# Optimization experiments

Measured on AMD Instinct MI355X. Metric: run time of the kernel, lower is better.

Reference implementation:

```python
import jax, jax.numpy as jnp
import numpy as np

MP_TIMES = 3  # mp_times from init


def setup_inputs() -> dict:
    key = jax.random.key(0)
    ks = jax.random.split(key, 16)
    N, E, F, EF = 10000, 50000, 32, 16
    DL, D, G, GD, OUT = 128, 64, 256, 8, 1

    def w(k, shape, fan_in):
        return jax.random.normal(k, shape, jnp.float32) / np.float32(np.sqrt(fan_in))

    return {
        "x": jax.random.normal(ks[0], (N, F), jnp.float32),
        "edge_index": jax.random.randint(ks[1], (2, E), 0, N),
        "edge_attr": jax.random.uniform(ks[2], (E, EF), jnp.float32),
        "batch": jax.random.randint(ks[3], (N,), 0, G),
        "graph_attr": jax.random.normal(ks[4], (G, GD), jnp.float32),
        # lin0
        "W0": w(ks[5], (D, F), F), "b0": jnp.zeros((D,), jnp.float32),
        # edge network MLP: EF -> DL -> D*D
        "We1": w(ks[6], (DL, EF), EF), "be1": jnp.zeros((DL,), jnp.float32),
        "We2": w(ks[7], (D * D, DL), DL), "be2": jnp.zeros((D * D,), jnp.float32),
        # NNConv root weight + bias
        "Wroot": w(ks[8], (D, D), D), "bconv": jnp.zeros((D,), jnp.float32),
        # GRU (torch gate order: r, z, n)
        "W_ih": w(ks[9], (3 * D, D), D), "W_hh": w(ks[10], (3 * D, D), D),
        "b_ih": jnp.zeros((3 * D,), jnp.float32), "b_hh": jnp.zeros((3 * D,), jnp.float32),
        # lin1 takes cat(node_state, graph_attr) -> D  (sized D+GD to make the source's cat runnable)
        "W1": w(ks[11], (D, D + GD), D + GD), "b1": jnp.zeros((D,), jnp.float32),
        # lin2
        "W2": w(ks[12], (OUT, D), D), "b2": jnp.zeros((OUT,), jnp.float32),
    }


def reference(x, edge_index, edge_attr, batch, graph_attr,
              W0, b0, We1, be1, We2, be2, Wroot, bconv,
              W_ih, W_hh, b_ih, b_hh, W1, b1, W2, b2):
    N = x.shape[0]
    D = W0.shape[0]
    src, dst = edge_index[0], edge_index[1]

    # Per-edge weight matrices from the edge MLP (loop-invariant: edge_attr is constant).
    ew = jnp.maximum(edge_attr @ We1.T + be1, 0.0) @ We2.T + be2  # [E, D*D]
    ew = ew.reshape(-1, D, D)                                      # [E, D, D]

    # mean-aggregation denominator (isolated nodes keep 0 via max(deg,1))
    deg = jax.ops.segment_sum(jnp.ones(src.shape[0], jnp.float32), dst, num_segments=N)
    denom = jnp.maximum(deg, 1.0)[:, None]                         # [N, 1]

    out = jnp.maximum(x @ W0.T + b0, 0.0)                          # [N, D]
    h = out
    for _ in range(MP_TIMES):
        # NNConv: gather -> per-edge matmul -> scatter-mean, plus root transform
        msg = jnp.einsum('ei,eio->eo', out[src], ew)               # [E, D]
        agg = jax.ops.segment_sum(msg, dst, num_segments=N) / denom
        m = jnp.maximum(agg + out @ Wroot.T + bconv, 0.0)          # [N, D]
        # single GRU step (torch GRUCell math, gate order r,z,n)
        gi = m @ W_ih.T + b_ih
        gh = h @ W_hh.T + b_hh
        i_r, i_z, i_n = jnp.split(gi, 3, axis=-1)
        h_r, h_z, h_n = jnp.split(gh, 3, axis=-1)
        r = jax.nn.sigmoid(i_r + h_r)
        z = jax.nn.sigmoid(i_z + h_z)
        n = jnp.tanh(i_n + r * h_n)
        h = (1.0 - z) * n + z * h
        out = h

    cat = jnp.concatenate([out, graph_attr[batch]], axis=-1)       # [N, D+GD]
    hid = jnp.maximum(cat @ W1.T + b1, 0.0)
    return hid @ W2.T + b2                                         # [N, dim_output]
```

## Files before the change

### kernel.cpp

```cpp
#include <hip/hip_runtime.h>
#include <hip/hip_bf16.h>
#include <math.h>

#define FIN 32
#define EFD 16
#define GDIM 8
#define ISPLIT 2

typedef __attribute__((ext_vector_type(8))) short short8;
typedef __attribute__((ext_vector_type(4))) float f32x4;

static __device__ __forceinline__ float bf2f(unsigned short u) {
  return __uint_as_float(((unsigned)u) << 16);
}
static __device__ __forceinline__ unsigned short f2bf(float f) {
  unsigned u = __float_as_uint(f);
  unsigned r = (u + 0x7FFFu + ((u >> 16) & 1u)) >> 16;
  return (unsigned short)r;
}

__global__ void zero_f32(float* __restrict__ p, int n) {
  int i = blockIdx.x * blockDim.x + threadIdx.x;
  if (i < n) p[i] = 0.0f;
}

__global__ void deg_kernel(const int* __restrict__ dst, float* __restrict__ deg, int E) {
  int e = blockIdx.x * blockDim.x + threadIdx.x;
  if (e < E) atomicAdd(&deg[dst[e]], 1.0f);
}

__global__ void setup_fused(const float* __restrict__ ea, const float* __restrict__ We1,
                            const float* __restrict__ be1, unsigned short* __restrict__ hidden,
                            const float* __restrict__ We2, unsigned short* __restrict__ We2f,
                            const float* __restrict__ Wroot, const float* __restrict__ W_hh,
                            const float* __restrict__ be2, const float* __restrict__ W_ih,
                            unsigned short* __restrict__ Wc_fh, unsigned short* __restrict__ Wc_fl,
                            unsigned short* __restrict__ Wih_fh, unsigned short* __restrict__ Wih_fl,
                            const float* __restrict__ x, const float* __restrict__ W0,
                            const float* __restrict__ b0, float* __restrict__ state,
                            int E, int N, int eB, int cB, int pB) {
  int b = blockIdx.x;
  if (b < eB) {
    int idx = b * 256 + threadIdx.x;
    int e = idx >> 7, l = idx & 127;
    if (e >= E) return;
    float acc = be1[l];
    const float* er = ea + (size_t)e * EFD;
    const float* wr = We1 + (size_t)l * EFD;
    #pragma unroll
    for (int j = 0; j < EFD; ++j) acc += er[j] * wr[j];
    hidden[idx] = f2bf(fmaxf(acc, 0.0f));
    return;
  }
  b -= eB;
  if (b < cB) {
    int fidx = b * 256 + threadIdx.x;
    if (fidx >= 4096 * 128) return;
    int j    = fidx & 7;
    int lane = (fidx >> 3) & 63;
    int kk   = (fidx >> 9) & 3;
    int wave = (fidx >> 11) & 3;
    int i    = fidx >> 13;
    int quad = lane >> 4, col = lane & 15;
    int row  = i * 64 + wave * 16 + col;
    int cw   = kk * 32 + quad * 8 + j;
    We2f[fidx] = f2bf(We2[(size_t)row * 128 + cw]);
    return;
  }
  b -= cB;
  if (b < pB) {
    int idx = b * 256 + threadIdx.x;
    if (idx >= 20480 + 12288) return;
    if (idx < 20480) {
      int j = idx & 7, lane = (idx >> 3) & 63, kk = (idx >> 9) & 1, cgk = idx >> 10;
      int quad = lane >> 4, mcol = lane & 15;
      int wave = cgk / 5, cg = cgk % 5;
      int c = wave * 80 + cg * 16 + mcol;
      int cw = kk * 32 + quad * 8 + j;
      float w;
      if (c < 64)       w = Wroot[c * 64 + cw];
      else if (c < 256) w = W_hh[(c - 64) * 64 + cw];
      else              w = be2[cw * 64 + (c - 256)];
      unsigned short h = f2bf(w);
      Wc_fh[idx] = h;
      Wc_fl[idx] = f2bf(w - bf2f(h));
    } else {
      int t = idx - 20480;
      int j = t & 7, lane = (t >> 3) & 63, kk = (t >> 9) & 1, gw = t >> 10;
      int quad = lane >> 4, mcol = lane & 15;
      int g = gw >> 2, wave = gw & 3;
      int row = g * 64 + wave * 16 + mcol;
      int cw = kk * 32 + quad * 8 + j;
      float w = W_ih[row * 64 + cw];
      unsigned short h = f2bf(w);
      Wih_fh[t] = h;
      Wih_fl[t] = f2bf(w - bf2f(h));
    }
    return;
  }
  b -= pB;
  {
    int idx = b * 256 + threadIdx.x;
    int n = idx >> 6, d = idx & 63;
    if (n >= N) return;
    float acc = b0[d];
    const float* xr = x + (size_t)n * FIN;
    const float* wr = W0 + (size_t)d * FIN;
    #pragma unroll
    for (int f = 0; f < FIN; ++f) acc += xr[f] * wr[f];
    state[idx] = fmaxf(acc, 0.0f);
  }
}

#define MFMA(A, B, C) __builtin_amdgcn_mfma_f32_16x16x32_bf16((A), (B), (C), 0, 0, 0)

__global__ __launch_bounds__(256) void pre_kernel(const float* __restrict__ state,
    const unsigned short* __restrict__ Wc_fh, const unsigned short* __restrict__ Wc_fl,
    float* __restrict__ R, int N) {
  __shared__ __align__(16) unsigned short Sh[32 * 72], Sl[32 * 72];
  int tid = threadIdx.x;
  int n0 = blockIdx.x * 32;
  {
    int nl = tid >> 3, part = tid & 7;
    int gn = n0 + nl;
    const float* sp = state + (size_t)gn * 64 + part * 8;
    #pragma unroll
    for (int j = 0; j < 2; ++j) {
      float4 v = make_float4(0.f, 0.f, 0.f, 0.f);
      if (gn < N) v = *(const float4*)(sp + j * 4);
      int base = nl * 72 + part * 8 + j * 4;
      unsigned short h;
      h = f2bf(v.x); Sh[base + 0] = h; Sl[base + 0] = f2bf(v.x - bf2f(h));
      h = f2bf(v.y); Sh[base + 1] = h; Sl[base + 1] = f2bf(v.y - bf2f(h));
      h = f2bf(v.z); Sh[base + 2] = h; Sl[base + 2] = f2bf(v.z - bf2f(h));
      h = f2bf(v.w); Sh[base + 3] = h; Sl[base + 3] = f2bf(v.w - bf2f(h));
    }
  }
  __syncthreads();
  int lane = tid & 63, wave = tid >> 6;
  int quad = lane >> 4, mcol = lane & 15;
  short8 ah[2][2], al[2][2];
  #pragma unroll
  for (int mt = 0; mt < 2; ++mt)
    #pragma unroll
    for (int kk = 0; kk < 2; ++kk) {
      ah[mt][kk] = *(const short8*)&Sh[(mt * 16 + mcol) * 72 + kk * 32 + quad * 8];
      al[mt][kk] = *(const short8*)&Sl[(mt * 16 + mcol) * 72 + kk * 32 + quad * 8];
    }
  int c0w = wave * 80;
  #pragma unroll 1
  for (int cg = 0; cg < 5; ++cg) {
    int c = c0w + cg * 16 + mcol;
    const unsigned short* bhp = Wc_fh + (size_t)(wave * 5 + cg) * 1024 + lane * 8;
    const unsigned short* blp = Wc_fl + (size_t)(wave * 5 + cg) * 1024 + lane * 8;
    short8 bh0 = *(const short8*)bhp, bh1 = *(const short8*)(bhp + 512);
    short8 bl0 = *(const short8*)blp, bl1 = *(const short8*)(blp + 512);
    #pragma unroll
    for (int mt = 0; mt < 2; ++mt) {
      f32x4 p = (f32x4){0.f, 0.f, 0.f, 0.f};
      p = MFMA(al[mt][0], bh0, p);
      p = MFMA(ah[mt][0], bl0, p);
      p = MFMA(ah[mt][0], bh0, p);
      p = MFMA(al[mt][1], bh1, p);
      p = MFMA(ah[mt][1], bl1, p);
      p = MFMA(ah[mt][1], bh1, p);
      #pragma unroll
      for (int r = 0; r < 4; ++r) {
        int row = n0 + mt * 16 + quad * 4 + r;
        if (row < N) R[(size_t)row * 320 + c] = p[r];
      }
    }
  }
}

__global__ __launch_bounds__(256) void msg_fused(const int* __restrict__ ei,
    const float* __restrict__ state, const unsigned short* __restrict__ hidden,
    const unsigned short* __restrict__ We2f, const float* __restrict__ R,
    float* __restrict__ agg, int E) {
  __shared__ __align__(16) char smem[64 * 136 * 2];
  __shared__ int srcs[64], dsts[64];
  unsigned short* Hs = (unsigned short*)smem;
  float* St = (float*)smem;
  int tid = threadIdx.x;
  int e0 = blockIdx.x * 64;
  int i0 = blockIdx.y * 32;
  if (tid < 64) {
    int e = e0 + tid;
    srcs[tid] = (e < E) ? ei[e] : -1;
    dsts[tid] = (e < E) ? ei[E + e] : -1;
  }
  {
    int er = tid >> 2, part = tid & 3;
    int ge = e0 + er;
    const unsigned short* hp = hidden + (size_t)ge * 128 + part * 32;
    #pragma unroll
    for (int j = 0; j < 4; ++j) {
      uint4 v = make_uint4(0u, 0u, 0u, 0u);
      if (ge < E) v = *(const uint4*)(hp + j * 8);
      *(uint4*)&Hs[er * 136 + part * 32 + j * 8] = v;
    }
  }
  __syncthreads();
  int lane = tid & 63, wave = tid >> 6;
  int n0 = wave * 16;
  int quad = lane >> 4, col = lane & 15;
  short8 a[4][4];
  #pragma unroll
  for (int mt = 0; mt < 4; ++mt)
    #pragma unroll
    for (int kk = 0; kk < 4; ++kk)
      a[mt][kk] = *(const short8*)&Hs[(mt * 16 + col) * 136 + kk * 32 + quad * 8];
  float4 sreg[2];
  {
    int sn = srcs[lane];
    const float* sp = state + (size_t)(sn < 0 ? 0 : sn) * 64 + i0 + wave * 8;
    #pragma unroll
    for (int j = 0; j < 2; ++j) {
      float4 v = make_float4(0.f, 0.f, 0.f, 0.f);
      if (sn >= 0) v = *(const float4*)(sp + j * 4);
      sreg[j] = v;
    }
  }
  __syncthreads();
  #pragma unroll
  for (int j = 0; j < 2; ++j) {
    int i = wave * 8 + j * 4;
    St[(i + 0) * 64 + lane] = sreg[j].x;
    St[(i + 1) * 64 + lane] = sreg[j].y;
    St[(i + 2) * 64 + lane] = sreg[j].z;
    St[(i + 3) * 64 + lane] = sreg[j].w;
  }
  __syncthreads();

  f32x4 macc0 = (f32x4){0.f,0.f,0.f,0.f}, macc1 = (f32x4){0.f,0.f,0.f,0.f};
  f32x4 macc2 = (f32x4){0.f,0.f,0.f,0.f}, macc3 = (f32x4){0.f,0.f,0.f,0.f};
  const unsigned short* bptr = We2f + (size_t)i0 * 8192 + wave * 2048 + lane * 8;
  short8 Xa = *(const short8*)(bptr + 0);
  short8 Xb = *(const short8*)(bptr + 512);
  short8 Xc = *(const short8*)(bptr + 1024);
  short8 Xd = *(const short8*)(bptr + 1536);
  short8 Ya, Yb, Yc, Yd;
  #pragma unroll 1
  for (int ii = 0; ii < 16; ++ii) {
    int i = ii * 2;
    {
      const unsigned short* bn = bptr + (size_t)(i + 1) * 8192;
      Ya = *(const short8*)(bn + 0);
      Yb = *(const short8*)(bn + 512);
      Yc = *(const short8*)(bn + 1024);
      Yd = *(const short8*)(bn + 1536);
    }
    {
      f32x4 sv0 = *(const f32x4*)&St[i * 64 +  0 + quad * 4];
      f32x4 sv1 = *(const f32x4*)&St[i * 64 + 16 + quad * 4];
      f32x4 sv2 = *(const f32x4*)&St[i * 64 + 32 + quad * 4];
      f32x4 sv3 = *(const f32x4*)&St[i * 64 + 48 + quad * 4];
      f32x4 p0 = (f32x4){0.f,0.f,0.f,0.f}, p1 = (f32x4){0.f,0.f,0.f,0.f};
      f32x4 p2 = (f32x4){0.f,0.f,0.f,0.f}, p3 = (f32x4){0.f,0.f,0.f,0.f};
      p0 = MFMA(a[0][0], Xa, p0); p1 = MFMA(a[1][0], Xa, p1);
      p2 = MFMA(a[2][0], Xa, p2); p3 = MFMA(a[3][0], Xa, p3);
      p0 = MFMA(a[0][1], Xb, p0); p1 = MFMA(a[1][1], Xb, p1);
      p2 = MFMA(a[2][1], Xb, p2); p3 = MFMA(a[3][1], Xb, p3);
      p0 = MFMA(a[0][2], Xc, p0); p1 = MFMA(a[1][2], Xc, p1);
      p2 = MFMA(a[2][2], Xc, p2); p3 = MFMA(a[3][2], Xc, p3);
      p0 = MFMA(a[0][3], Xd, p0); p1 = MFMA(a[1][3], Xd, p1);
      p2 = MFMA(a[2][3], Xd, p2); p3 = MFMA(a[3][3], Xd, p3);
      macc0 += sv0 * p0; macc1 += sv1 * p1; macc2 += sv2 * p2; macc3 += sv3 * p3;
    }
    if (ii < 15) {
      const unsigned short* bn = bptr + (size_t)(i + 2) * 8192;
      Xa = *(const short8*)(bn + 0);
      Xb = *(const short8*)(bn + 512);
      Xc = *(const short8*)(bn + 1024);
      Xd = *(const short8*)(bn + 1536);
    }
    {
      int io = i + 1;
      f32x4 sv0 = *(const f32x4*)&St[io * 64 +  0 + quad * 4];
      f32x4 sv1 = *(const f32x4*)&St[io * 64 + 16 + quad * 4];
      f32x4 sv2 = *(const f32x4*)&St[io * 64 + 32 + quad * 4];
      f32x4 sv3 = *(const f32x4*)&St[io * 64 + 48 + quad * 4];
      f32x4 p0 = (f32x4){0.f,0.f,0.f,0.f}, p1 = (f32x4){0.f,0.f,0.f,0.f};
      f32x4 p2 = (f32x4){0.f,0.f,0.f,0.f}, p3 = (f32x4){0.f,0.f,0.f,0.f};
      p0 = MFMA(a[0][0], Ya, p0); p1 = MFMA(a[1][0], Ya, p1);
      p2 = MFMA(a[2][0], Ya, p2); p3 = MFMA(a[3][0], Ya, p3);
      p0 = MFMA(a[0][1], Yb, p0); p1 = MFMA(a[1][1], Yb, p1);
      p2 = MFMA(a[2][1], Yb, p2); p3 = MFMA(a[3][1], Yb, p3);
      p0 = MFMA(a[0][2], Yc, p0); p1 = MFMA(a[1][2], Yc, p1);
      p2 = MFMA(a[2][2], Yc, p2); p3 = MFMA(a[3][2], Yc, p3);
      p0 = MFMA(a[0][3], Yd, p0); p1 = MFMA(a[1][3], Yd, p1);
      p2 = MFMA(a[2][3], Yd, p2); p3 = MFMA(a[3][3], Yd, p3);
      macc0 += sv0 * p0; macc1 += sv1 * p1; macc2 += sv2 * p2; macc3 += sv3 * p3;
    }
  }
  int addu = (blockIdx.y == 0);
  f32x4 maccA[4] = {macc0, macc1, macc2, macc3};
  #pragma unroll
  for (int mt = 0; mt < 4; ++mt) {
    #pragma unroll
    for (int r = 0; r < 4; ++r) {
      int el = mt * 16 + quad * 4 + r;
      int d = dsts[el];
      if (d >= 0) {
        float val = maccA[mt][r];
        if (addu) val += R[(size_t)srcs[el] * 320 + 256 + n0 + col];
        atomicAdd(&agg[(size_t)d * 64 + n0 + col], val);
      }
    }
  }
}

__global__ __launch_bounds__(256) void gate_pre(float* __restrict__ agg,
    const float* __restrict__ deg, float* __restrict__ state,
    float* __restrict__ R, const float* __restrict__ bconv,
    const unsigned short* __restrict__ Wih_fh, const unsigned short* __restrict__ Wih_fl,
    const float* __restrict__ b_ih, const float* __restrict__ b_hh,
    const unsigned short* __restrict__ Wc_fh, const unsigned short* __restrict__ Wc_fl,
    int N, int do_pre) {
  __shared__ __align__(16) unsigned short Mh[32 * 72], Ml[32 * 72];
  int tid = threadIdx.x;
  int n0 = blockIdx.x * 32;
  {
    int nl = tid >> 3, part = tid & 7;
    int gn = n0 + nl;
    float inv = 1.0f;
    if (gn < N) inv = 1.0f / fmaxf(deg[gn], 1.0f);
    #pragma unroll
    for (int j = 0; j < 2; ++j) {
      int o = part * 8 + j * 4;
      float4 av = make_float4(0.f, 0.f, 0.f, 0.f);
      float4 rv = make_float4(0.f, 0.f, 0.f, 0.f);
      if (gn < N) {
        av = *(const float4*)(agg + (size_t)gn * 64 + o);
        rv = *(const float4*)(R + (size_t)gn * 320 + o);
      }
      float4 bv = *(const float4*)(bconv + o);
      float m0 = fmaxf(av.x * inv + rv.x + bv.x, 0.0f);
      float m1 = fmaxf(av.y * inv + rv.y + bv.y, 0.0f);
      float m2 = fmaxf(av.z * inv + rv.z + bv.z, 0.0f);
      float m3 = fmaxf(av.w * inv + rv.w + bv.w, 0.0f);
      int base = nl * 72 + o;
      unsigned short h;
      h = f2bf(m0); Mh[base + 0] = h; Ml[base + 0] = f2bf(m0 - bf2f(h));
      h = f2bf(m1); Mh[base + 1] = h; Ml[base + 1] = f2bf(m1 - bf2f(h));
      h = f2bf(m2); Mh[base + 2] = h; Ml[base + 2] = f2bf(m2 - bf2f(h));
      h = f2bf(m3); Mh[base + 3] = h; Ml[base + 3] = f2bf(m3 - bf2f(h));
      if (gn < N)
        *(float4*)(agg + (size_t)gn * 64 + o) = make_float4(0.f, 0.f, 0.f, 0.f);
    }
  }
  __syncthreads();
  int lane = tid & 63, wave = tid >> 6;
  int quad = lane >> 4, mcol = lane & 15;
  short8 ah[2][2], al[2][2];
  #pragma unroll
  for (int mt = 0; mt < 2; ++mt)
    #pragma unroll
    for (int kk = 0; kk < 2; ++kk) {
      ah[mt][kk] = *(const short8*)&Mh[(mt * 16 + mcol) * 72 + kk * 32 + quad * 8];
      al[mt][kk] = *(const short8*)&Ml[(mt * 16 + mcol) * 72 + kk * 32 + quad * 8];
    }
  int c = wave * 16 + mcol;
  f32x4 accg[3][2];
  #pragma unroll 1
  for (int g = 0; g < 3; ++g) {
    const unsigned short* bhp = Wih_fh + (size_t)g * 4096 + wave * 1024 + lane * 8;
    const unsigned short* blp = Wih_fl + (size_t)g * 4096 + wave * 1024 + lane * 8;
    short8 bh0 = *(const short8*)bhp, bh1 = *(const short8*)(bhp + 512);
    short8 bl0 = *(const short8*)blp, bl1 = *(const short8*)(blp + 512);
    #pragma unroll
    for (int mt = 0; mt < 2; ++mt) {
      f32x4 p = (f32x4){0.f, 0.f, 0.f, 0.f};
      p = MFMA(al[mt][0], bh0, p);
      p = MFMA(ah[mt][0], bl0, p);
      p = MFMA(ah[mt][0], bh0, p);
      p = MFMA(al[mt][1], bh1, p);
      p = MFMA(ah[mt][1], bl1, p);
      p = MFMA(ah[mt][1], bh1, p);
      accg[g][mt] = p;
    }
  }
  float bir = b_ih[c], biz = b_ih[64 + c], bin = b_ih[128 + c];
  float bhr = b_hh[c], bhz = b_hh[64 + c], bhn = b_hh[128 + c];
  float hnew[2][4];
  #pragma unroll
  for (int mt = 0; mt < 2; ++mt) {
    #pragma unroll
    for (int r = 0; r < 4; ++r) {
      int node = n0 + mt * 16 + quad * 4 + r;
      hnew[mt][r] = 0.0f;
      if (node >= N) continue;
      const float* Rn = R + (size_t)node * 320;
      float gir = accg[0][mt][r] + bir + Rn[64 + c] + bhr;
      float giz = accg[1][mt][r] + biz + Rn[128 + c] + bhz;
      float ghn = Rn[192 + c] + bhn;
      float rg = 1.0f / (1.0f + expf(-gir));
      float zg = 1.0f / (1.0f + expf(-giz));
      float ng = tanhf(accg[2][mt][r] + bin + rg * ghn);
      size_t si = (size_t)node * 64 + c;
      float h = state[si];
      float hv = (1.0f - zg) * ng + zg * h;
      state[si] = hv;
      hnew[mt][r] = hv;
    }
  }
  if (!do_pre) return;
  __syncthreads();
  #pragma unroll
  for (int mt = 0; mt < 2; ++mt) {
    #pragma unroll
    for (int r = 0; r < 4; ++r) {
      int base = (mt * 16 + quad * 4 + r) * 72 + c;
      float v = hnew[mt][r];
      unsigned short h = f2bf(v);
      Mh[base] = h; Ml[base] = f2bf(v - bf2f(h));
    }
  }
  __syncthreads();
  short8 ph[2][2], pl[2][2];
  #pragma unroll
  for (int mt = 0; mt < 2; ++mt)
    #pragma unroll
    for (int kk = 0; kk < 2; ++kk) {
      ph[mt][kk] = *(const short8*)&Mh[(mt * 16 + mcol) * 72 + kk * 32 + quad * 8];
      pl[mt][kk] = *(const short8*)&Ml[(mt * 16 + mcol) * 72 + kk * 32 + quad * 8];
    }
  #pragma unroll 1
  for (int cg = 0; cg < 5; ++cg) {
    int cc = wave * 80 + cg * 16 + mcol;
    const unsigned short* bhp = Wc_fh + (size_t)(wave * 5 + cg) * 1024 + lane * 8;
    const unsigned short* blp = Wc_fl + (size_t)(wave * 5 + cg) * 1024 + lane * 8;
    short8 bh0 = *(const short8*)bhp, bh1 = *(const short8*)(bhp + 512);
    short8 bl0 = *(const short8*)blp, bl1 = *(const short8*)(blp + 512);
    #pragma unroll
    for (int mt = 0; mt < 2; ++mt) {
      f32x4 p = (f32x4){0.f, 0.f, 0.f, 0.f};
      p = MFMA(pl[mt][0], bh0, p);
      p = MFMA(ph[mt][0], bl0, p);
      p = MFMA(ph[mt][0], bh0, p);
      p = MFMA(pl[mt][1], bh1, p);
      p = MFMA(ph[mt][1], bl1, p);
      p = MFMA(ph[mt][1], bh1, p);
      #pragma unroll
      for (int r = 0; r < 4; ++r) {
        int row = n0 + mt * 16 + quad * 4 + r;
        if (row < N) R[(size_t)row * 320 + cc] = p[r];
      }
    }
  }
}

__global__ __launch_bounds__(256) void final_kernel(const float* __restrict__ state,
    const int* __restrict__ batch, const float* __restrict__ gattr,
    const float* __restrict__ W1, const float* __restrict__ b1,
    const float* __restrict__ W2, const float* __restrict__ b2,
    float* __restrict__ out, int N) {
  int lane = threadIdx.x & 63;
  int n = blockIdx.x * 4 + (threadIdx.x >> 6);
  if (n >= N) return;
  float s = state[(size_t)n * 64 + lane];
  int b = batch[n];
  float acc = b1[lane];
  const float* w = W1 + (size_t)lane * 72;
  for (int i = 0; i < 64; ++i) acc += __shfl(s, i) * w[i];
  const float* gar = gattr + (size_t)b * GDIM;
  #pragma unroll
  for (int j = 0; j < GDIM; ++j) acc += gar[j] * w[64 + j];
  float hid = fmaxf(acc, 0.0f);
  float v = hid * W2[lane];
  #pragma unroll
  for (int off = 32; off > 0; off >>= 1) v += __shfl_xor(v, off);
  if (lane == 0) out[n] = v + b2[0];
}

extern "C" void kernel_launch(void* const* d_in, const int* in_sizes, int n_in,
                              void* d_out, int out_size, void* d_ws, size_t ws_size,
                              hipStream_t stream) {
  const float* x     = (const float*)d_in[0];
  const int*   ei    = (const int*)d_in[1];
  const float* ea    = (const float*)d_in[2];
  const int*   batch = (const int*)d_in[3];
  const float* ga    = (const float*)d_in[4];
  const float* W0    = (const float*)d_in[5];
  const float* b0    = (const float*)d_in[6];
  const float* We1   = (const float*)d_in[7];
  const float* be1   = (const float*)d_in[8];
  const float* We2   = (const float*)d_in[9];
  const float* be2   = (const float*)d_in[10];
  const float* Wroot = (const float*)d_in[11];
  const float* bconv = (const float*)d_in[12];
  const float* W_ih  = (const float*)d_in[13];
  const float* W_hh  = (const float*)d_in[14];
  const float* b_ih  = (const float*)d_in[15];
  const float* b_hh  = (const float*)d_in[16];
  const float* W1    = (const float*)d_in[17];
  const float* b1    = (const float*)d_in[18];
  const float* W2    = (const float*)d_in[19];
  const float* b2    = (const float*)d_in[20];
  int N = in_sizes[0] / FIN;
  int E = in_sizes[1] / 2;
  float* out = (float*)d_out;

  char* p = (char*)d_ws;
  float* state = (float*)p; p += (size_t)N * 64 * 4;
  float* agg   = (float*)p; p += (size_t)N * 64 * 4;
  float* deg   = (float*)p; p += ((size_t)N * 4 + 15) & ~(size_t)15;
  float* R     = (float*)p; p += (size_t)N * 320 * 4;
  unsigned short* hidden = (unsigned short*)p; p += (size_t)E * 128 * 2;
  unsigned short* We2f   = (unsigned short*)p; p += (size_t)4096 * 128 * 2;
  unsigned short* Wc_fh  = (unsigned short*)p; p += 320 * 64 * 2;
  unsigned short* Wc_fl  = (unsigned short*)p; p += 320 * 64 * 2;
  unsigned short* Wih_fh = (unsigned short*)p; p += 192 * 64 * 2;
  unsigned short* Wih_fl = (unsigned short*)p; p += 192 * 64 * 2;

  int tileBlocks = (N + 31) / 32;
  int edgeBlocks = (E + 63) / 64;

  int eB = (E * 128 + 255) / 256;
  int cB = (4096 * 128 + 255) / 256;
  int pB = (32768 + 255) / 256;
  int lB = (N * 64 + 255) / 256;

  zero_f32<<<(N * 65 + 255) / 256, 256, 0, stream>>>(agg, N * 65);
  deg_kernel<<<(E + 255) / 256, 256, 0, stream>>>(ei + E, deg, E);
  setup_fused<<<eB + cB + pB + lB, 256, 0, stream>>>(
      ea, We1, be1, hidden, We2, We2f, Wroot, W_hh, be2, W_ih,
      Wc_fh, Wc_fl, Wih_fh, Wih_fl, x, W0, b0, state, E, N, eB, cB, pB);
  pre_kernel<<<tileBlocks, 256, 0, stream>>>(state, Wc_fh, Wc_fl, R, N);
  for (int t = 0; t < 3; ++t) {
    dim3 mg(edgeBlocks, ISPLIT);
    msg_fused<<<mg, 256, 0, stream>>>(ei, state, hidden, We2f, R, agg, E);
    gate_pre<<<tileBlocks, 256, 0, stream>>>(agg, deg, state, R, bconv,
                                             Wih_fh, Wih_fl, b_ih, b_hh,
                                             Wc_fh, Wc_fl, N, (t < 2) ? 1 : 0);
  }
  final_kernel<<<(N + 3) / 4, 256, 0, stream>>>(state, batch, ga, W1, b1, W2, b2, out, N);
}
```

Baseline: 422.3 us.

## Issue all global loads in msg_fused before one barrier and interleave split blocks

The msg_fused prologue now issues the src-index, gathered state, hidden-tile and first two We2 weight-slice loads together before writing shared memory. This replaces two barriers with a single one by giving Hs and St separate LDS buffers. The Y-weight prefetch moves to the end of each loop iteration so it overlaps the next iteration's MFMAs. The grid is flattened so the two i-split halves of each edge tile run in adjacent blocks, which may improve L2 reuse of the hidden/state gathers. The cost is more LDS per block and higher register pressure, both of which may lower occupancy.

```diff
diff --git a/kernel.cpp b/kernel.cpp
--- a/kernel.cpp
+++ b/kernel.cpp
@@ -177,51 +177,55 @@
     const float* __restrict__ state, const unsigned short* __restrict__ hidden,
     const unsigned short* __restrict__ We2f, const float* __restrict__ R,
     float* __restrict__ agg, int E) {
-  __shared__ __align__(16) char smem[64 * 136 * 2];
+  __shared__ __align__(16) unsigned short Hs[64 * 136];
+  __shared__ __align__(16) float St[32 * 64];
   __shared__ int srcs[64], dsts[64];
-  unsigned short* Hs = (unsigned short*)smem;
-  float* St = (float*)smem;
   int tid = threadIdx.x;
-  int e0 = blockIdx.x * 64;
-  int i0 = blockIdx.y * 32;
+  int bx = blockIdx.x >> 1;
+  int by = blockIdx.x & 1;
+  int e0 = bx * 64;
+  int i0 = by * 32;
+  int lane = tid & 63, wave = tid >> 6;
+  int eL = e0 + lane;
+  int snL = (eL < E) ? ei[eL] : -1;
   if (tid < 64) {
-    int e = e0 + tid;
-    srcs[tid] = (e < E) ? ei[e] : -1;
-    dsts[tid] = (e < E) ? ei[E + e] : -1;
-  }
+    srcs[tid] = snL;
+    dsts[tid] = (eL < E) ? ei[E + eL] : -1;
+  }
+  float4 sreg[2];
   {
-    int er = tid >> 2, part = tid & 3;
-    int ge = e0 + er;
+    const float* sp = state + (size_t)(snL < 0 ? 0 : snL) * 64 + i0 + wave * 8;
+    #pragma unroll
+    for (int j = 0; j < 2; ++j) {
+      float4 v = make_float4(0.f, 0.f, 0.f, 0.f);
+      if (snL >= 0) v = *(const float4*)(sp + j * 4);
+      sreg[j] = v;
+    }
+  }
+  int er = tid >> 2, part = tid & 3;
+  int ge = e0 + er;
+  uint4 hv[4];
+  {
     const unsigned short* hp = hidden + (size_t)ge * 128 + part * 32;
     #pragma unroll
     for (int j = 0; j < 4; ++j) {
       uint4 v = make_uint4(0u, 0u, 0u, 0u);
       if (ge < E) v = *(const uint4*)(hp + j * 8);
-      *(uint4*)&Hs[er * 136 + part * 32 + j * 8] = v;
-    }
-  }
-  __syncthreads();
-  int lane = tid & 63, wave = tid >> 6;
-  int n0 = wave * 16;
-  int quad = lane >> 4, col = lane & 15;
-  short8 a[4][4];
-  #pragma unroll
-  for (int mt = 0; mt < 4; ++mt)
-    #pragma unroll
-    for (int kk = 0; kk < 4; ++kk)
-      a[mt][kk] = *(const short8*)&Hs[(mt * 16 + col) * 136 + kk * 32 + quad * 8];
-  float4 sreg[2];
-  {
-    int sn = srcs[lane];
-    const float* sp = state + (size_t)(sn < 0 ? 0 : sn) * 64 + i0 + wave * 8;
-    #pragma unroll
-    for (int j = 0; j < 2; ++j) {
-      float4 v = make_float4(0.f, 0.f, 0.f, 0.f);
-      if (sn >= 0) v = *(const float4*)(sp + j * 4);
-      sreg[j] = v;
-    }
-  }
-  __syncthreads();
+      hv[j] = v;
+    }
+  }
+  const unsigned short* bptr = We2f + (size_t)i0 * 8192 + wave * 2048 + lane * 8;
+  short8 Xa = *(const short8*)(bptr + 0);
+  short8 Xb = *(const short8*)(bptr + 512);
+  short8 Xc = *(const short8*)(bptr + 1024);
+  short8 Xd = *(const short8*)(bptr + 1536);
+  short8 Ya = *(const short8*)(bptr + 8192 + 0);
+  short8 Yb = *(const short8*)(bptr + 8192 + 512);
+  short8 Yc = *(const short8*)(bptr + 8192 + 1024);
+  short8 Yd = *(const short8*)(bptr + 8192 + 1536);
+  #pragma unroll
+  for (int j = 0; j < 4; ++j)
+    *(uint4*)&Hs[er * 136 + part * 32 + j * 8] = hv[j];
   #pragma unroll
   for (int j = 0; j < 2; ++j) {
     int i = wave * 8 + j * 4;
@@ -231,25 +235,20 @@
     St[(i + 3) * 64 + lane] = sreg[j].w;
   }
   __syncthreads();
+  int n0 = wave * 16;
+  int quad = lane >> 4, col = lane & 15;
+  short8 a[4][4];
+  #pragma unroll
+  for (int mt = 0; mt < 4; ++mt)
+    #pragma unroll
+    for (int kk = 0; kk < 4; ++kk)
+      a[mt][kk] = *(const short8*)&Hs[(mt * 16 + col) * 136 + kk * 32 + quad * 8];
 
   f32x4 macc0 = (f32x4){0.f,0.f,0.f,0.f}, macc1 = (f32x4){0.f,0.f,0.f,0.f};
   f32x4 macc2 = (f32x4){0.f,0.f,0.f,0.f}, macc3 = (f32x4){0.f,0.f,0.f,0.f};
-  const unsigned short* bptr = We2f + (size_t)i0 * 8192 + wave * 2048 + lane * 8;
-  short8 Xa = *(const short8*)(bptr + 0);
-  short8 Xb = *(const short8*)(bptr + 512);
-  short8 Xc = *(const short8*)(bptr + 1024);
-  short8 Xd = *(const short8*)(bptr + 1536);
-  short8 Ya, Yb, Yc, Yd;
   #pragma unroll 1
   for (int ii = 0; ii < 16; ++ii) {
     int i = ii * 2;
-    {
-      const unsigned short* bn = bptr + (size_t)(i + 1) * 8192;
-      Ya = *(const short8*)(bn + 0);
-      Yb = *(const short8*)(bn + 512);
-      Yc = *(const short8*)(bn + 1024);
-      Yd = *(const short8*)(bn + 1536);
-    }
     {
       f32x4 sv0 = *(const f32x4*)&St[i * 64 +  0 + quad * 4];
       f32x4 sv1 = *(const f32x4*)&St[i * 64 + 16 + quad * 4];
@@ -292,8 +291,15 @@
       p2 = MFMA(a[2][3], Yd, p2); p3 = MFMA(a[3][3], Yd, p3);
       macc0 += sv0 * p0; macc1 += sv1 * p1; macc2 += sv2 * p2; macc3 += sv3 * p3;
     }
-  }
-  int addu = (blockIdx.y == 0);
+    if (ii < 15) {
+      const unsigned short* bn = bptr + (size_t)(i + 3) * 8192;
+      Ya = *(const short8*)(bn + 0);
+      Yb = *(const short8*)(bn + 512);
+      Yc = *(const short8*)(bn + 1024);
+      Yd = *(const short8*)(bn + 1536);
+    }
+  }
+  int addu = (by == 0);
   f32x4 maccA[4] = {macc0, macc1, macc2, macc3};
   #pragma unroll
   for (int mt = 0; mt < 4; ++mt) {
@@ -528,8 +534,7 @@
       Wc_fh, Wc_fl, Wih_fh, Wih_fl, x, W0, b0, state, E, N, eB, cB, pB);
   pre_kernel<<<tileBlocks, 256, 0, stream>>>(state, Wc_fh, Wc_fl, R, N);
   for (int t = 0; t < 3; ++t) {
-    dim3 mg(edgeBlocks, ISPLIT);
-    msg_fused<<<mg, 256, 0, stream>>>(ei, state, hidden, We2f, R, agg, E);
+    msg_fused<<<edgeBlocks * ISPLIT, 256, 0, stream>>>(ei, state, hidden, We2f, R, agg, E);
     gate_pre<<<tileBlocks, 256, 0, stream>>>(agg, deg, state, R, bconv,
                                              Wih_fh, Wih_fl, b_ih, b_hh,
                                              Wc_fh, Wc_fl, N, (t < 2) ? 1 : 0);
```

After: 450.0 us. +6.6%, slower.
